# Kernel optimization log

Measured on AMD Instinct MI355X. Metric: run time of the kernel, lower is better.

Reference implementation:

```python
import jax, jax.numpy as jnp
import numpy as np

B, S, H = 32, 2048, 1024

def setup_inputs() -> dict:
    key = jax.random.key(0)
    ks = jax.random.split(key, 8)
    sc = 1.0 / np.sqrt(H)
    return {
        "decoder_hidden": jax.random.normal(ks[0], (B, H), jnp.float32),
        "encoder_outputs": jax.random.normal(ks[1], (B, S, H), jnp.float32),
        "mask": jax.random.randint(ks[2], (B, S), 0, 2, jnp.int32),
        "Wa_w": jax.random.normal(ks[3], (H, H), jnp.float32) * sc,
        "Wa_b": jax.random.normal(ks[4], (H,), jnp.float32) * sc,
        "Ua_w": jax.random.normal(ks[5], (H, H), jnp.float32) * sc,
        "Ua_b": jax.random.normal(ks[6], (H,), jnp.float32) * sc,
        "Va_w": jax.random.normal(ks[7], (H,), jnp.float32) * sc,
        "Va_b": jnp.float32(0.0),
    }

def reference(decoder_hidden, encoder_outputs, mask, Wa_w, Wa_b, Ua_w, Ua_b, Va_w, Va_b):
    # dec proj: [B,H] -> [B,1,H]; enc proj: [B,S,H]
    dec_proj = (decoder_hidden @ Wa_w + Wa_b)[:, None, :]
    enc_proj = jnp.einsum('bsh,hk->bsk', encoder_outputs, Ua_w) + Ua_b
    energy = jnp.tanh(dec_proj + enc_proj)                      # [B,S,H]
    scores = jnp.einsum('bsh,h->bs', energy, Va_w) + Va_b       # [B,S]
    scores = jnp.where(mask == 0, jnp.float32(-1e9), scores)
    return jax.nn.softmax(scores, axis=1)
```

## Files before the change

kernel.cpp:

```cpp
#include <hip/hip_runtime.h>
#include <math.h>

#define BB 32
#define SS 2048
#define HH 1024
#define MT (BB*SS)

#define BM 128
#define BN 256
#define BK 32
#define NT (HH/BK)
#define NCH (HH/BN)
#define THREADS 512
#define BTILE 16384

typedef float  f32x4 __attribute__((ext_vector_type(4)));
typedef short  s16x8 __attribute__((ext_vector_type(8)));
typedef unsigned short u16;

__device__ inline void split1(float x, u16& h, u16& l) {
    unsigned u = __float_as_uint(x);
    h = (u16)(u >> 16);
    float hf = __uint_as_float((u >> 16) << 16);
    l = (u16)(__float_as_uint(x - hf) >> 16);
}
__device__ inline void split8v(float4 v0, float4 v1, s16x8& h, s16x8& l) {
    float x[8] = {v0.x,v0.y,v0.z,v0.w,v1.x,v1.y,v1.z,v1.w};
    #pragma unroll
    for (int j = 0; j < 8; ++j) {
        u16 hh, ll; split1(x[j], hh, ll);
        h[j] = (short)hh; l[j] = (short)ll;
    }
}

__global__ void dec_proj_kernel(const float* __restrict__ dh,
                                const float* __restrict__ Wa_w,
                                const float* __restrict__ Wa_b,
                                const float* __restrict__ Ua_b,
                                float* __restrict__ dec_proj) {
    __shared__ float sdh[HH];
    const int b   = blockIdx.x;
    const int nq  = blockIdx.y;
    const int tid = threadIdx.x;
    for (int i = tid; i < HH; i += 256) sdh[i] = dh[b*HH + i];
    __syncthreads();
    const int n = nq*256 + tid;
    float acc = Wa_b[n] + Ua_b[n];
    for (int k = 0; k < HH; ++k)
        acc = fmaf(sdh[k], Wa_w[(size_t)k*HH + n], acc);
    dec_proj[b*HH + n] = acc;
}

__global__ void transpose_convert_kernel(const float* __restrict__ Ua,
                                         u16* __restrict__ B_pre) {
    __shared__ u16 shh[64][72], shl[64][72];
    const int nb = blockIdx.x * 64, kb = blockIdx.y * 64;
    const int tid = threadIdx.x;
    const int kl = tid >> 4, nl4 = (tid & 15) * 4;
    #pragma unroll
    for (int q = 0; q < 4; ++q) {
        const int k = kl + q*16;
        float4 v = *(const float4*)&Ua[(size_t)(kb + k)*HH + nb + nl4];
        float x[4] = {v.x, v.y, v.z, v.w};
        #pragma unroll
        for (int j = 0; j < 4; ++j) {
            u16 hh, ll; split1(x[j], hh, ll);
            shh[k][nl4 + j] = hh; shl[k][nl4 + j] = ll;
        }
    }
    __syncthreads();
    const int nl = tid >> 3, kc8 = (tid & 7) * 8;
    #pragma unroll
    for (int q = 0; q < 2; ++q) {
        const int n = nb + nl + q*32;
        const int kglob = kb + kc8;
        s16x8 hv, lv;
        #pragma unroll
        for (int j = 0; j < 8; ++j) {
            hv[j] = (short)shh[kc8 + j][nl + q*32];
            lv[j] = (short)shl[kc8 + j][nl + q*32];
        }
        const int nchI = n >> 8, fI = (n >> 4) & 15, lrI = n & 15;
        const int ktI = kglob >> 5, cI = (kglob >> 3) & 3;
        const size_t base = (size_t)(nchI*NT + ktI) * BTILE;
        const size_t idxH = base + fI*512 + (cI*16 + lrI)*8;
        *(s16x8*)&B_pre[idxH]        = hv;
        *(s16x8*)&B_pre[idxH + 8192] = lv;
    }
}

__global__ __launch_bounds__(THREADS, 4)
void gemm_fr_kernel(const float* __restrict__ A,
                    const u16* __restrict__ B_pre,
                    const float* __restrict__ dec_proj,
                    const float* __restrict__ Va_w,
                    float* __restrict__ partials)
{
    __shared__ __align__(16) u16 AhS[2][BM*BK];
    __shared__ __align__(16) u16 AlS[2][BM*BK];

    const int bid = blockIdx.x;
    const int wg  = (bid & 7) * 256 + (bid >> 3);
    const int nch = wg & 3;
    const int mt  = wg >> 2;
    const int m0  = mt * BM, n0 = nch * BN;

    const int tid = threadIdx.x, lane = tid & 63, wid = tid >> 6;
    const int wm = wid >> 2, wn = wid & 3;
    const int lr = lane & 15, lk = lane >> 4;

    const float* Ab = A + (size_t)(m0 + (tid>>6)*16 + (tid&15))*HH + ((tid>>4)&3)*8;
    const int awoff = tid*8;
    const u16* Bt = B_pre + (size_t)nch*NT*BTILE + (wn*4)*512 + lane*8;

    f32x4 acc[4][4];
    #pragma unroll
    for (int i = 0; i < 4; ++i)
        #pragma unroll
        for (int j = 0; j < 4; ++j) acc[i][j] = (f32x4){0.f,0.f,0.f,0.f};

    s16x8  bh[4], bl[4];
    float4 a0_, a1_;

    auto loadA = [&](int kt) {
        const float* p = Ab + kt*BK;
        a0_ = *(const float4*)(p + 0);
        a1_ = *(const float4*)(p + 4);
    };
    auto writeA = [&](int db) {
        s16x8 h, l;
        split8v(a0_, a1_, h, l);
        *(s16x8*)&AhS[db][awoff] = h;
        *(s16x8*)&AlS[db][awoff] = l;
    };
    auto readB = [&](int kt) {
        const u16* p = Bt + (size_t)kt*BTILE;
        #pragma unroll
        for (int j = 0; j < 4; ++j) {
            bh[j] = *(const s16x8*)(p + j*512);
            bl[j] = *(const s16x8*)(p + 8192 + j*512);
        }
    };

    loadA(0);
    writeA(0);
    readB(0);
    __syncthreads();
    loadA(1);

    for (int j = 0; j < NT; ++j) {
        const int cb = j & 1;
        const bool hn = (j + 1 < NT);

        #pragma unroll
        for (int f = 0; f < 4; ++f) {
            const int o = (wm*4 + f)*512 + lane*8;
            const s16x8 ah = *(const s16x8*)&AhS[cb][o];
            const s16x8 al = *(const s16x8*)&AlS[cb][o];
            __builtin_amdgcn_s_setprio(1);
            #pragma unroll
            for (int q = 0; q < 4; ++q) {
                f32x4 c = acc[f][q];
                c = __builtin_amdgcn_mfma_f32_16x16x32_bf16(ah, bh[q], c, 0, 0, 0);
                c = __builtin_amdgcn_mfma_f32_16x16x32_bf16(ah, bl[q], c, 0, 0, 0);
                c = __builtin_amdgcn_mfma_f32_16x16x32_bf16(al, bh[q], c, 0, 0, 0);
                acc[f][q] = c;
            }
            __builtin_amdgcn_s_setprio(0);
        }
        if (hn) {
            readB(j + 1);
            writeA(cb ^ 1);
            loadA(j + 2 < NT ? j + 2 : j + 1);
        }
        asm volatile("s_waitcnt lgkmcnt(0)" ::: "memory");
        __builtin_amdgcn_sched_barrier(0);
        __builtin_amdgcn_s_barrier();
        __builtin_amdgcn_sched_barrier(0);
    }

    const int bidx = m0 >> 11;
    float dp[4], va[4];
    #pragma unroll
    for (int j = 0; j < 4; ++j) {
        const int n = n0 + wn*64 + j*16 + lr;
        dp[j] = dec_proj[bidx*HH + n];
        va[j] = Va_w[n];
    }
    #pragma unroll
    for (int f = 0; f < 4; ++f) {
        #pragma unroll
        for (int r = 0; r < 4; ++r) {
            float s = 0.f;
            #pragma unroll
            for (int j = 0; j < 4; ++j)
                s += va[j] * tanhf(acc[f][j][r] + dp[j]);
            s += __shfl_xor(s, 1, 64);
            s += __shfl_xor(s, 2, 64);
            s += __shfl_xor(s, 4, 64);
            s += __shfl_xor(s, 8, 64);
            if (lr == 0) {
                const int m = m0 + wm*64 + f*16 + lk*4 + r;
                partials[(size_t)m*16 + nch*4 + wn] = s;
            }
        }
    }
}

__global__ void softmax_kernel(const float* __restrict__ partials,
                               const int* __restrict__ mask,
                               const float* __restrict__ vb_ptr,
                               float* __restrict__ out)
{
    const int b   = blockIdx.x;
    const int tid = threadIdx.x;
    __shared__ float sred[8];
    const float vb = vb_ptr[0];
    float sc[8];
    float mymax = -INFINITY;
    #pragma unroll
    for (int i = 0; i < 8; ++i) {
        const int s = i*256 + tid;
        const float4* p = (const float4*)&partials[((size_t)b*SS + s)*16];
        const float4 x = p[0], y = p[1], z = p[2], w = p[3];
        float v = (((x.x+x.y)+(x.z+x.w)) + ((y.x+y.y)+(y.z+y.w)))
                + (((z.x+z.y)+(z.z+z.w)) + ((w.x+w.y)+(w.z+w.w))) + vb;
        if (mask[b*SS + s] == 0) v = -1e9f;
        sc[i] = v;
        mymax = fmaxf(mymax, v);
    }
    #pragma unroll
    for (int off = 1; off < 64; off <<= 1)
        mymax = fmaxf(mymax, __shfl_xor(mymax, off, 64));
    const int wave = tid >> 6, lane = tid & 63;
    if (lane == 0) sred[wave] = mymax;
    __syncthreads();
    const float bmax = fmaxf(fmaxf(sred[0], sred[1]), fmaxf(sred[2], sred[3]));
    float ex[8], mysum = 0.f;
    #pragma unroll
    for (int i = 0; i < 8; ++i) {
        ex[i] = __expf(sc[i] - bmax);
        mysum += ex[i];
    }
    #pragma unroll
    for (int off = 1; off < 64; off <<= 1)
        mysum += __shfl_xor(mysum, off, 64);
    if (lane == 0) sred[4 + wave] = mysum;
    __syncthreads();
    const float inv = 1.f / (sred[4] + sred[5] + sred[6] + sred[7]);
    #pragma unroll
    for (int i = 0; i < 8; ++i)
        out[(size_t)b*SS + i*256 + tid] = ex[i] * inv;
}

extern "C" void kernel_launch(void* const* d_in, const int* in_sizes, int n_in,
                              void* d_out, int out_size, void* d_ws, size_t ws_size,
                              hipStream_t stream) {
    const float* dh   = (const float*)d_in[0];
    const float* enc  = (const float*)d_in[1];
    const int*   mask = (const int*)d_in[2];
    const float* Wa_w = (const float*)d_in[3];
    const float* Wa_b = (const float*)d_in[4];
    const float* Ua_w = (const float*)d_in[5];
    const float* Ua_b = (const float*)d_in[6];
    const float* Va_w = (const float*)d_in[7];
    const float* Va_b = (const float*)d_in[8];
    float* out = (float*)d_out;

    float* dec_proj = (float*)d_ws;
    float* partials = dec_proj + BB*HH;
    u16*   B_pre    = (u16*)(partials + (size_t)MT*16);

    dec_proj_kernel<<<dim3(BB, 4), 256, 0, stream>>>(dh, Wa_w, Wa_b, Ua_b, dec_proj);
    transpose_convert_kernel<<<dim3(HH/64, HH/64), 256, 0, stream>>>(Ua_w, B_pre);
    gemm_fr_kernel<<<(MT/BM)*NCH, THREADS, 0, stream>>>(enc, B_pre, dec_proj, Va_w, partials);
    softmax_kernel<<<BB, 256, 0, stream>>>(partials, mask, Va_b, out);
}
```

Before: 393.7 us.

## Double M tile to 256 and interleave loads across four barrier phases

The GEMM block tile grows from 128 to 256 rows, so each wave computes 8x4 MFMA fragments and reuses each B fragment twice. B fragments are now double-buffered in registers. The prefetch work (B read, A split/write, A global load) is spread across four sub-phases per K step, each with its own barriers, instead of being bunched at the end. This trades more accumulators and registers (launch bounds drop to 2 blocks per SM) and more barriers for less B traffic per FLOP and better overlap.

```diff
diff --git a/kernel.cpp b/kernel.cpp
--- a/kernel.cpp
+++ b/kernel.cpp
@@ -6,7 +6,7 @@
 #define HH 1024
 #define MT (BB*SS)
 
-#define BM 128
+#define BM 256
 #define BN 256
 #define BK 32
 #define NT (HH/BK)
@@ -89,8 +89,8 @@
     }
 }
 
-__global__ __launch_bounds__(THREADS, 4)
-void gemm_fr_kernel(const float* __restrict__ A,
+__global__ __launch_bounds__(THREADS, 2)
+void gemm_8p_kernel(const float* __restrict__ A,
                     const u16* __restrict__ B_pre,
                     const float* __restrict__ dec_proj,
                     const float* __restrict__ Va_w,
@@ -100,7 +100,7 @@
     __shared__ __align__(16) u16 AlS[2][BM*BK];
 
     const int bid = blockIdx.x;
-    const int wg  = (bid & 7) * 256 + (bid >> 3);
+    const int wg  = (bid & 7) * 128 + (bid >> 3);
     const int nch = wg & 3;
     const int mt  = wg >> 2;
     const int m0  = mt * BM, n0 = nch * BN;
@@ -109,74 +109,90 @@
     const int wm = wid >> 2, wn = wid & 3;
     const int lr = lane & 15, lk = lane >> 4;
 
-    const float* Ab = A + (size_t)(m0 + (tid>>6)*16 + (tid&15))*HH + ((tid>>4)&3)*8;
-    const int awoff = tid*8;
+    const int e0 = tid, e1 = tid + 512;
+    const float* Ab0 = A + (size_t)(m0 + (e0>>6)*16 + (e0&15))*HH + ((e0>>4)&3)*8;
+    const float* Ab1 = A + (size_t)(m0 + (e1>>6)*16 + (e1&15))*HH + ((e1>>4)&3)*8;
+    const int aw0 = tid*8, aw1 = tid*8 + 4096;
     const u16* Bt = B_pre + (size_t)nch*NT*BTILE + (wn*4)*512 + lane*8;
 
-    f32x4 acc[4][4];
-    #pragma unroll
-    for (int i = 0; i < 4; ++i)
+    f32x4 acc[8][4];
+    #pragma unroll
+    for (int i = 0; i < 8; ++i)
         #pragma unroll
         for (int j = 0; j < 4; ++j) acc[i][j] = (f32x4){0.f,0.f,0.f,0.f};
 
-    s16x8  bh[4], bl[4];
-    float4 a0_, a1_;
+    s16x8 bhA[4], blA[4], bhB[4], blB[4];
+    float4 a0_, a1_, a2_, a3_;
 
     auto loadA = [&](int kt) {
-        const float* p = Ab + kt*BK;
-        a0_ = *(const float4*)(p + 0);
-        a1_ = *(const float4*)(p + 4);
+        const float* p0 = Ab0 + kt*BK;
+        const float* p1 = Ab1 + kt*BK;
+        a0_ = *(const float4*)(p0 + 0);
+        a1_ = *(const float4*)(p0 + 4);
+        a2_ = *(const float4*)(p1 + 0);
+        a3_ = *(const float4*)(p1 + 4);
     };
     auto writeA = [&](int db) {
         s16x8 h, l;
         split8v(a0_, a1_, h, l);
-        *(s16x8*)&AhS[db][awoff] = h;
-        *(s16x8*)&AlS[db][awoff] = l;
-    };
-    auto readB = [&](int kt) {
+        *(s16x8*)&AhS[db][aw0] = h; *(s16x8*)&AlS[db][aw0] = l;
+        split8v(a2_, a3_, h, l);
+        *(s16x8*)&AhS[db][aw1] = h; *(s16x8*)&AlS[db][aw1] = l;
+    };
+    auto readB = [&](int kt, s16x8 (&bh)[4], s16x8 (&bl)[4]) {
         const u16* p = Bt + (size_t)kt*BTILE;
         #pragma unroll
-        for (int j = 0; j < 4; ++j) {
-            bh[j] = *(const s16x8*)(p + j*512);
-            bl[j] = *(const s16x8*)(p + 8192 + j*512);
-        }
-    };
-
-    loadA(0);
-    writeA(0);
-    readB(0);
-    __syncthreads();
-    loadA(1);
-
-    for (int j = 0; j < NT; ++j) {
-        const int cb = j & 1;
+        for (int q = 0; q < 4; ++q) {
+            bh[q] = *(const s16x8*)(p + q*512);
+            bl[q] = *(const s16x8*)(p + 8192 + q*512);
+        }
+    };
+
+    auto tile = [&](int j, s16x8 (&Bch)[4], s16x8 (&Bcl)[4],
+                           s16x8 (&Bnh)[4], s16x8 (&Bnl)[4]) {
+        const int  cb = j & 1;
         const bool hn = (j + 1 < NT);
-
-        #pragma unroll
-        for (int f = 0; f < 4; ++f) {
-            const int o = (wm*4 + f)*512 + lane*8;
-            const s16x8 ah = *(const s16x8*)&AhS[cb][o];
-            const s16x8 al = *(const s16x8*)&AlS[cb][o];
+        #pragma unroll
+        for (int p = 0; p < 4; ++p) {
+            const int f0 = (wm*8 + p*2)*512 + lane*8;
+            s16x8 ah0 = *(const s16x8*)&AhS[cb][f0];
+            s16x8 al0 = *(const s16x8*)&AlS[cb][f0];
+            s16x8 ah1 = *(const s16x8*)&AhS[cb][f0 + 512];
+            s16x8 al1 = *(const s16x8*)&AlS[cb][f0 + 512];
+            if (p == 0 && hn) readB(j + 1, Bnh, Bnl);
+            if (p == 1 && hn) writeA(cb ^ 1);
+            if (p == 2 && j + 2 < NT) loadA(j + 2);
+            __builtin_amdgcn_s_barrier();
+            asm volatile("s_waitcnt lgkmcnt(0)" ::: "memory");
+            __builtin_amdgcn_sched_barrier(0);
             __builtin_amdgcn_s_setprio(1);
             #pragma unroll
             for (int q = 0; q < 4; ++q) {
-                f32x4 c = acc[f][q];
-                c = __builtin_amdgcn_mfma_f32_16x16x32_bf16(ah, bh[q], c, 0, 0, 0);
-                c = __builtin_amdgcn_mfma_f32_16x16x32_bf16(ah, bl[q], c, 0, 0, 0);
-                c = __builtin_amdgcn_mfma_f32_16x16x32_bf16(al, bh[q], c, 0, 0, 0);
-                acc[f][q] = c;
+                f32x4 c0 = acc[p*2 + 0][q];
+                c0 = __builtin_amdgcn_mfma_f32_16x16x32_bf16(ah0, Bch[q], c0, 0, 0, 0);
+                c0 = __builtin_amdgcn_mfma_f32_16x16x32_bf16(ah0, Bcl[q], c0, 0, 0, 0);
+                c0 = __builtin_amdgcn_mfma_f32_16x16x32_bf16(al0, Bch[q], c0, 0, 0, 0);
+                acc[p*2 + 0][q] = c0;
+                f32x4 c1 = acc[p*2 + 1][q];
+                c1 = __builtin_amdgcn_mfma_f32_16x16x32_bf16(ah1, Bch[q], c1, 0, 0, 0);
+                c1 = __builtin_amdgcn_mfma_f32_16x16x32_bf16(ah1, Bcl[q], c1, 0, 0, 0);
+                c1 = __builtin_amdgcn_mfma_f32_16x16x32_bf16(al1, Bch[q], c1, 0, 0, 0);
+                acc[p*2 + 1][q] = c1;
             }
             __builtin_amdgcn_s_setprio(0);
-        }
-        if (hn) {
-            readB(j + 1);
-            writeA(cb ^ 1);
-            loadA(j + 2 < NT ? j + 2 : j + 1);
-        }
-        asm volatile("s_waitcnt lgkmcnt(0)" ::: "memory");
-        __builtin_amdgcn_sched_barrier(0);
-        __builtin_amdgcn_s_barrier();
-        __builtin_amdgcn_sched_barrier(0);
+            __builtin_amdgcn_s_barrier();
+        }
+    };
+
+    loadA(0);
+    writeA(0);
+    readB(0, bhA, blA);
+    __syncthreads();
+    loadA(1);
+
+    for (int j2 = 0; j2 < NT; j2 += 2) {
+        tile(j2,     bhA, blA, bhB, blB);
+        tile(j2 + 1, bhB, blB, bhA, blA);
     }
 
     const int bidx = m0 >> 11;
@@ -188,7 +204,7 @@
         va[j] = Va_w[n];
     }
     #pragma unroll
-    for (int f = 0; f < 4; ++f) {
+    for (int f = 0; f < 8; ++f) {
         #pragma unroll
         for (int r = 0; r < 4; ++r) {
             float s = 0.f;
@@ -200,7 +216,7 @@
             s += __shfl_xor(s, 4, 64);
             s += __shfl_xor(s, 8, 64);
             if (lr == 0) {
-                const int m = m0 + wm*64 + f*16 + lk*4 + r;
+                const int m = m0 + wm*128 + f*16 + lk*4 + r;
                 partials[(size_t)m*16 + nch*4 + wn] = s;
             }
         }
@@ -273,6 +289,6 @@
 
     dec_proj_kernel<<<dim3(BB, 4), 256, 0, stream>>>(dh, Wa_w, Wa_b, Ua_b, dec_proj);
     transpose_convert_kernel<<<dim3(HH/64, HH/64), 256, 0, stream>>>(Ua_w, B_pre);
-    gemm_fr_kernel<<<(MT/BM)*NCH, THREADS, 0, stream>>>(enc, B_pre, dec_proj, Va_w, partials);
+    gemm_8p_kernel<<<(MT/BM)*NCH, THREADS, 0, stream>>>(enc, B_pre, dec_proj, Va_w, partials);
     softmax_kernel<<<BB, 256, 0, stream>>>(partials, mask, Va_b, out);
 }
```

After: 554.6 us. +40.9%, slower.
